# Optimization experiments

Measured on AMD Instinct MI355X. Metric: run time of the kernel, lower is better.

## Reference

```python
import jax, jax.numpy as jnp
import numpy as np


def setup_inputs() -> dict:
    key = jax.random.key(0)
    k1, k2, k3, k4, k5 = jax.random.split(key, 5)
    B, H, W, C = 4, 64, 64, 256
    d = C // 8
    return {
        "x": jax.random.normal(k1, (B, H, W, C), dtype=jnp.float32),
        "Wf": jax.random.normal(k2, (C, d), dtype=jnp.float32) * 0.05,
        "Wg": jax.random.normal(k3, (C, d), dtype=jnp.float32) * 0.05,
        "Wh": jax.random.normal(k4, (C, C), dtype=jnp.float32) * 0.05,
        "gamma": jax.random.normal(k5, (1,), dtype=jnp.float32),
    }


def reference(x, Wf, Wg, Wh, gamma):
    # x: [B,H,W,C]; 1x1 convs (no bias) == channel matmuls
    B, H, W, C = x.shape
    N = H * W
    f = jnp.einsum('bhwc,cd->bhwd', x, Wf).reshape(B, N, -1)  # keys  [B,N,d]
    g = jnp.einsum('bhwc,cd->bhwd', x, Wg).reshape(B, N, -1)  # query [B,N,d]
    h = jnp.einsum('bhwc,ce->bhwe', x, Wh).reshape(B, N, -1)  # value [B,N,C]
    s = jnp.einsum('bnd,bmd->bnm', g, f)       # [B,N,N], no 1/sqrt(d) scale (faithful)
    beta = jax.nn.softmax(s, axis=-1)
    o = jnp.einsum('bnm,bmc->bnc', beta, h).reshape(B, H, W, C)
    return gamma * o + x
```

## Files before the change

kernel.cpp:

```cpp
#include <hip/hip_runtime.h>
#include <math.h>

#define B_   4
#define N_   4096
#define C_   256
#define D_   32
#define QT   64
#define KTB  128
#define NT2  (N_/KTB)
#define L2E  1.4426950408889634f

typedef __attribute__((ext_vector_type(8)))  short  short8;
typedef __attribute__((ext_vector_type(4)))  float  f32x4;
typedef __attribute__((ext_vector_type(16))) float  f32x16;

__device__ __forceinline__ unsigned short f2bf(float f) {
    unsigned int u = __builtin_bit_cast(unsigned int, f);
    u += 0x7fffu + ((u >> 16) & 1u);
    return (unsigned short)(u >> 16);
}
__device__ __forceinline__ unsigned pack2(float lo, float hi) {
    return (unsigned)f2bf(lo) | ((unsigned)f2bf(hi) << 16);
}
__device__ __forceinline__ unsigned pack2rn(float lo, float hi) {
    unsigned ul = __builtin_bit_cast(unsigned, lo) + 0x8000u;
    unsigned uh = __builtin_bit_cast(unsigned, hi) + 0x8000u;
    return (ul >> 16) | (uh & 0xffff0000u);
}

__global__ __launch_bounds__(64) void wcast(const float* __restrict__ Wf,
        const float* __restrict__ Wg, const float* __restrict__ Wh,
        unsigned short* __restrict__ WT) {
    const int e = blockIdx.x;
    const int t = threadIdx.x;
    const float* src; int stride, col; float sc = 1.f;
    if (e < 256)      { src = Wh; stride = 256; col = e; }
    else if (e < 288) { src = Wf; stride = 32;  col = e - 256; }
    else              { src = Wg; stride = 32;  col = e - 288; sc = L2E; }
    const int c0 = t * 4;
    __align__(8) unsigned short tmp[4];
    #pragma unroll
    for (int i = 0; i < 4; ++i)
        tmp[i] = f2bf(src[(size_t)(c0 + i) * stride + col] * sc);
    *(uint2*)(WT + (size_t)e * 256 + c0) = *(const uint2*)tmp;
}

__global__ __launch_bounds__(256, 2) void proj(const float* __restrict__ x,
        const unsigned short* __restrict__ WT,
        unsigned short* __restrict__ f, unsigned short* __restrict__ g,
        unsigned short* __restrict__ hT) {
    __shared__ unsigned short xb[32 * 256];
    const int t = threadIdx.x;
    const int l = t & 63, w = t >> 6;
    const long n0 = (long)blockIdx.x * 32;
    const int b = (int)(n0 >> 12), nloc = (int)(n0 & 4095);

    {
        const int r = t >> 3, ch = (t & 7) * 32;
        const float* xp = x + (n0 + r) * C_ + ch;
        #pragma unroll
        for (int m4 = 0; m4 < 8; ++m4) {
            float4 v = *(const float4*)(xp + m4 * 4);
            unsigned u0 = pack2(v.x, v.y), u1 = pack2(v.z, v.w);
            const int byte = (r * 512 + (ch + m4 * 4) * 2) ^ ((r & 7) << 4);
            *(uint2*)((char*)xb + byte) = make_uint2(u0, u1);
        }
    }
    __syncthreads();

    const int l15 = l & 15, l31 = l & 31;
    const int l4 = (l >> 4) & 3, hi = (l >> 5) & 1;

    f32x16 acc0, acc1;
    #pragma unroll
    for (int i = 0; i < 16; ++i) { acc0[i] = 0.f; acc1[i] = 0.f; }
    const int e0 = w * 64 + l31;
    #pragma unroll
    for (int ks = 0; ks < 16; ++ks) {
        short8 A = *(const short8*)((const char*)xb +
                    ((l31 * 512 + ks * 32 + hi * 16) ^ ((l31 & 7) << 4)));
        short8 B0 = *(const short8*)(WT + (size_t)e0 * 256 + ks * 16 + hi * 8);
        short8 B1 = *(const short8*)(WT + (size_t)(e0 + 32) * 256 + ks * 16 + hi * 8);
        acc0 = __builtin_amdgcn_mfma_f32_32x32x16_bf16(A, B0, acc0, 0, 0, 0);
        acc1 = __builtin_amdgcn_mfma_f32_32x32x16_bf16(A, B1, acc1, 0, 0, 0);
    }
    f32x4 fgacc[2];
    #pragma unroll
    for (int rf = 0; rf < 2; ++rf)
        #pragma unroll
        for (int i = 0; i < 4; ++i) fgacc[rf][i] = 0.f;
    const int fcol = w * 16 + l15;
    #pragma unroll
    for (int ks2 = 0; ks2 < 8; ++ks2) {
        short8 Bf = *(const short8*)(WT + (size_t)(256 + fcol) * 256 + ks2 * 32 + l4 * 8);
        #pragma unroll
        for (int rf = 0; rf < 2; ++rf) {
            const int row = rf * 16 + l15;
            short8 A = *(const short8*)((const char*)xb +
                        ((row * 512 + ks2 * 64 + l4 * 16) ^ ((row & 7) << 4)));
            fgacc[rf] = __builtin_amdgcn_mfma_f32_16x16x32_bf16(A, Bf, fgacc[rf], 0, 0, 0);
        }
    }

    #pragma unroll
    for (int ef = 0; ef < 2; ++ef) {
        const f32x16& a = ef ? acc1 : acc0;
        const int e = e0 + ef * 32;
        unsigned short* dp = hT + ((size_t)b * C_ + e) * N_ + nloc + 4 * hi;
        #pragma unroll
        for (int qd = 0; qd < 4; ++qd) {
            unsigned u0 = pack2(a[4*qd+0], a[4*qd+1]);
            unsigned u1 = pack2(a[4*qd+2], a[4*qd+3]);
            *(uint2*)(dp + 8 * qd) = make_uint2(u0, u1);
        }
    }
    {
        unsigned short* outp = (fcol < 32) ? (f + fcol) : (g + fcol - 32);
        #pragma unroll
        for (int rf = 0; rf < 2; ++rf)
            #pragma unroll
            for (int r = 0; r < 4; ++r) {
                const int row = rf * 16 + l4 * 4 + r;
                outp[(size_t)(n0 + row) * D_] = f2bf(fgacc[rf][r]);
            }
    }
}

__global__ __launch_bounds__(512, 2) void attn(
        const unsigned short* __restrict__ g,
        const unsigned short* __restrict__ f,
        const unsigned short* __restrict__ hT,
        const float* __restrict__ x,
        const float* __restrict__ gammap,
        float* __restrict__ out) {

    __shared__ unsigned short P[2][QT * KTB];
    __shared__ float Lpart[8][4][16];
    __shared__ float linv[QT];

    const int bid = (int)blockIdx.x;
    const int s = (bid & 7) * 32 + (bid >> 3);
    const int q0 = (s & 63) * QT;
    const int b  = s >> 6;

    const int t = threadIdx.x, l = t & 63, w = t >> 6;
    const long nb = (long)b * N_;
    const unsigned short* hb = hT + (size_t)b * C_ * N_;

    {
        uint4* pz = (uint4*)&P[0][0];
        pz[t] = make_uint4(0,0,0,0);       pz[t+512]  = make_uint4(0,0,0,0);
        pz[t+1024] = make_uint4(0,0,0,0);  pz[t+1536] = make_uint4(0,0,0,0);
    }

    const int l15 = l & 15, l31 = l & 31;
    const int l4 = (l >> 4) & 3, hi = (l >> 5) & 1;

    short8 gB[4];
    #pragma unroll
    for (int qf = 0; qf < 4; ++qf)
        gB[qf] = *(const short8*)(g + (size_t)(nb + q0 + qf*16 + l15) * D_ + l4*8);

    const int ecol = w * 32 + l31;
    const unsigned short* hcol = hb + (size_t)ecol * N_ + hi * 8;
    const size_t fbase = (size_t)(nb + w*16 + l15) * D_ + l4*8;

    const int pwB = ((w*2 + (l4>>1))*64 + l15)*16 + (l4&1)*8;
    const int prB = hi*1024 + l31*16;

    float la[4] = {0.f, 0.f, 0.f, 0.f};
    f32x16 acc0, acc1;
    #pragma unroll
    for (int i = 0; i < 16; ++i) { acc0[i] = 0.f; acc1[i] = 0.f; }

    short8 fA[2], hB[2][8];
    fA[0] = *(const short8*)(f + fbase);
    fA[1] = *(const short8*)(f + fbase + (size_t)KTB * D_);
    #pragma unroll
    for (int kk = 0; kk < 8; ++kk) {
        hB[0][kk] = *(const short8*)(hcol + kk * 16);
        hB[1][kk] = *(const short8*)(hcol + (size_t)KTB + kk * 16);
    }

    f32x4 S[4];

#define QK(slot) { \
    f32x4 zz; zz[0]=0.f; zz[1]=0.f; zz[2]=0.f; zz[3]=0.f; \
    _Pragma("unroll") \
    for (int qf = 0; qf < 4; ++qf) \
        S[qf] = __builtin_amdgcn_mfma_f32_16x16x32_bf16(fA[slot], gB[qf], zz, 0,0,0); \
}

#define EXPAND(buf) { \
    _Pragma("unroll") \
    for (int qf = 0; qf < 4; ++qf) { \
        float p0 = exp2f(S[qf][0]); \
        float p1 = exp2f(S[qf][1]); \
        float p2 = exp2f(S[qf][2]); \
        float p3 = exp2f(S[qf][3]); \
        la[qf] += (p0+p1)+(p2+p3); \
        *(uint2*)((char*)&P[buf][0] + pwB + qf*256) = \
            make_uint2(pack2rn(p0,p1), pack2rn(p2,p3)); \
    } \
}

#define BODY(CUR, NXT, kvar, DO_N, DO_PF) { \
    __syncthreads(); \
    if (DO_N) QK(NXT); \
    _Pragma("unroll") \
    for (int kk = 0; kk < 8; ++kk) { \
        short8 a0 = *(const short8*)((const char*)&P[CUR][0] + kk*2048 + prB); \
        short8 a1 = *(const short8*)((const char*)&P[CUR][0] + kk*2048 + prB + 512); \
        acc0 = __builtin_amdgcn_mfma_f32_32x32x16_bf16(a0, hB[CUR][kk], acc0, 0,0,0); \
        acc1 = __builtin_amdgcn_mfma_f32_32x32x16_bf16(a1, hB[CUR][kk], acc1, 0,0,0); \
    } \
    if (DO_PF) { \
        const int ktp = ((kvar) + 2) & (NT2 - 1); \
        fA[CUR] = *(const short8*)(f + fbase + (size_t)ktp * KTB * D_); \
        _Pragma("unroll") \
        for (int kk = 0; kk < 8; ++kk) \
            hB[CUR][kk] = *(const short8*)(hcol + (size_t)ktp * KTB + kk * 16); \
    } \
    if (DO_N) EXPAND(NXT); \
}

    QK(0);
    __syncthreads();
    EXPAND(0);

    #pragma unroll 1
    for (int k = 0; k < NT2 - 2; k += 2) {
        BODY(0, 1, k,     true, true);
        BODY(1, 0, k + 1, true, true);
    }
    BODY(0, 1, NT2 - 2, true,  false);
    BODY(1, 0, NT2 - 1, false, false);
#undef BODY
#undef EXPAND
#undef QK

    #pragma unroll
    for (int qf = 0; qf < 4; ++qf) {
        la[qf] += __shfl_xor(la[qf], 16, 64);
        la[qf] += __shfl_xor(la[qf], 32, 64);
    }
    if (l < 16) {
        #pragma unroll
        for (int qf = 0; qf < 4; ++qf) Lpart[w][qf][l] = la[qf];
    }
    __syncthreads();
    if (t < QT) {
        const int qf = t >> 4, r = t & 15;
        float sm = 0.f;
        #pragma unroll
        for (int ww = 0; ww < 8; ++ww) sm += Lpart[ww][qf][r];
        linv[t] = 1.f / fmaxf(sm, 1e-30f);
    }
    __syncthreads();

    const float gamma = gammap[0];
    #pragma unroll
    for (int qh = 0; qh < 2; ++qh) {
        const f32x16& a = qh ? acc1 : acc0;
        #pragma unroll
        for (int reg = 0; reg < 16; ++reg) {
            const int row = qh*32 + (reg & 3) + 8*(reg >> 2) + 4*hi;
            const size_t o = (size_t)(nb + q0 + row) * C_ + ecol;
            out[o] = fmaf(gamma, a[reg] * linv[row], x[o]);
        }
    }
}

extern "C" void kernel_launch(void* const* d_in, const int* in_sizes, int n_in,
                              void* d_out, int out_size, void* d_ws, size_t ws_size,
                              hipStream_t stream) {
    const float* x     = (const float*)d_in[0];
    const float* Wf    = (const float*)d_in[1];
    const float* Wg    = (const float*)d_in[2];
    const float* Wh    = (const float*)d_in[3];
    const float* gamma = (const float*)d_in[4];
    float* out = (float*)d_out;

    unsigned short* WT  = (unsigned short*)d_ws;
    unsigned short* fb  = WT + 320 * 256;
    unsigned short* gb  = fb + (size_t)B_ * N_ * D_;
    unsigned short* hTb = gb + (size_t)B_ * N_ * D_;

    wcast<<<dim3(320), dim3(64), 0, stream>>>(Wf, Wg, Wh, WT);
    proj <<<dim3(B_ * N_ / 32), dim3(256), 0, stream>>>(x, WT, fb, gb, hTb);
    attn <<<dim3(256), dim3(512), 0, stream>>>(gb, fb, hTb, x, gamma, out);
}
```

Baseline: 95.37 us.

## Split attention work across 16 waves with single-buffered V prefetch

Doubles the attention block to 1024 threads so each wave handles half the query rows (2 q-fragments, one 32x32 accumulator) for its column slice. The V tile prefetch becomes single-buffered, issued one tile ahead, while keys stay two tiles ahead. The aim is to cut per-wave register pressure and raise wave-level parallelism for latency hiding. In exchange, each V column is loaded by two waves, and V-load latency is less hidden.

```diff
diff --git a/kernel.cpp b/kernel.cpp
--- a/kernel.cpp
+++ b/kernel.cpp
@@ -126,7 +126,7 @@
     }
 }
 
-__global__ __launch_bounds__(512, 2) void attn(
+__global__ __launch_bounds__(1024, 4) void attn(
         const unsigned short* __restrict__ g,
         const unsigned short* __restrict__ f,
         const unsigned short* __restrict__ hT,
@@ -135,7 +135,7 @@
         float* __restrict__ out) {
 
     __shared__ unsigned short P[2][QT * KTB];
-    __shared__ float Lpart[8][4][16];
+    __shared__ float Lpart[16][2][16];
     __shared__ float linv[QT];
 
     const int bid = (int)blockIdx.x;
@@ -149,125 +149,119 @@
 
     {
         uint4* pz = (uint4*)&P[0][0];
-        pz[t] = make_uint4(0,0,0,0);       pz[t+512]  = make_uint4(0,0,0,0);
-        pz[t+1024] = make_uint4(0,0,0,0);  pz[t+1536] = make_uint4(0,0,0,0);
+        pz[t] = make_uint4(0,0,0,0);
+        pz[t + 1024] = make_uint4(0,0,0,0);
     }
 
     const int l15 = l & 15, l31 = l & 31;
     const int l4 = (l >> 4) & 3, hi = (l >> 5) & 1;
-
-    short8 gB[4];
-    #pragma unroll
-    for (int qf = 0; qf < 4; ++qf)
-        gB[qf] = *(const short8*)(g + (size_t)(nb + q0 + qf*16 + l15) * D_ + l4*8);
-
-    const int ecol = w * 32 + l31;
+    const int kf = w & 7;
+    const int qp = (w >> 3) * 2;
+    const int qh = w >> 3;
+
+    short8 gB[2];
+    #pragma unroll
+    for (int j = 0; j < 2; ++j)
+        gB[j] = *(const short8*)(g + (size_t)(nb + q0 + (qp+j)*16 + l15) * D_ + l4*8);
+
+    const int ecol = (w & 7) * 32 + l31;
     const unsigned short* hcol = hb + (size_t)ecol * N_ + hi * 8;
-    const size_t fbase = (size_t)(nb + w*16 + l15) * D_ + l4*8;
-
-    const int pwB = ((w*2 + (l4>>1))*64 + l15)*16 + (l4&1)*8;
-    const int prB = hi*1024 + l31*16;
-
-    float la[4] = {0.f, 0.f, 0.f, 0.f};
-    f32x16 acc0, acc1;
-    #pragma unroll
-    for (int i = 0; i < 16; ++i) { acc0[i] = 0.f; acc1[i] = 0.f; }
-
-    short8 fA[2], hB[2][8];
-    fA[0] = *(const short8*)(f + fbase);
-    fA[1] = *(const short8*)(f + fbase + (size_t)KTB * D_);
-    #pragma unroll
-    for (int kk = 0; kk < 8; ++kk) {
-        hB[0][kk] = *(const short8*)(hcol + kk * 16);
-        hB[1][kk] = *(const short8*)(hcol + (size_t)KTB + kk * 16);
-    }
-
-    f32x4 S[4];
-
-#define QK(slot) { \
+    const size_t fbase = (size_t)(nb + kf*16 + l15) * D_ + l4*8;
+
+    const int pwB = ((kf*2 + (l4>>1))*64 + l15)*16 + (l4&1)*8 + qp*256;
+    const int prB = hi*1024 + qh*512 + l31*16;
+
+    float la0 = 0.f, la1 = 0.f;
+    f32x16 acc;
+    #pragma unroll
+    for (int i = 0; i < 16; ++i) acc[i] = 0.f;
+
+    short8 fA, hB[8];
+    fA = *(const short8*)(f + fbase);
+    #pragma unroll
+    for (int kk = 0; kk < 8; ++kk)
+        hB[kk] = *(const short8*)(hcol + kk * 16);
+
+    f32x4 S[2];
+
+#define QK() { \
     f32x4 zz; zz[0]=0.f; zz[1]=0.f; zz[2]=0.f; zz[3]=0.f; \
-    _Pragma("unroll") \
-    for (int qf = 0; qf < 4; ++qf) \
-        S[qf] = __builtin_amdgcn_mfma_f32_16x16x32_bf16(fA[slot], gB[qf], zz, 0,0,0); \
+    S[0] = __builtin_amdgcn_mfma_f32_16x16x32_bf16(fA, gB[0], zz, 0,0,0); \
+    S[1] = __builtin_amdgcn_mfma_f32_16x16x32_bf16(fA, gB[1], zz, 0,0,0); \
 }
 
 #define EXPAND(buf) { \
-    _Pragma("unroll") \
-    for (int qf = 0; qf < 4; ++qf) { \
-        float p0 = exp2f(S[qf][0]); \
-        float p1 = exp2f(S[qf][1]); \
-        float p2 = exp2f(S[qf][2]); \
-        float p3 = exp2f(S[qf][3]); \
-        la[qf] += (p0+p1)+(p2+p3); \
-        *(uint2*)((char*)&P[buf][0] + pwB + qf*256) = \
+    { \
+        float p0 = exp2f(S[0][0]), p1 = exp2f(S[0][1]); \
+        float p2 = exp2f(S[0][2]), p3 = exp2f(S[0][3]); \
+        la0 += (p0+p1)+(p2+p3); \
+        *(uint2*)((char*)&P[buf][0] + pwB) = \
+            make_uint2(pack2rn(p0,p1), pack2rn(p2,p3)); \
+    } \
+    { \
+        float p0 = exp2f(S[1][0]), p1 = exp2f(S[1][1]); \
+        float p2 = exp2f(S[1][2]), p3 = exp2f(S[1][3]); \
+        la1 += (p0+p1)+(p2+p3); \
+        *(uint2*)((char*)&P[buf][0] + pwB + 256) = \
             make_uint2(pack2rn(p0,p1), pack2rn(p2,p3)); \
     } \
 }
 
 #define BODY(CUR, NXT, kvar, DO_N, DO_PF) { \
     __syncthreads(); \
-    if (DO_N) QK(NXT); \
+    if (DO_N) QK(); \
     _Pragma("unroll") \
     for (int kk = 0; kk < 8; ++kk) { \
-        short8 a0 = *(const short8*)((const char*)&P[CUR][0] + kk*2048 + prB); \
-        short8 a1 = *(const short8*)((const char*)&P[CUR][0] + kk*2048 + prB + 512); \
-        acc0 = __builtin_amdgcn_mfma_f32_32x32x16_bf16(a0, hB[CUR][kk], acc0, 0,0,0); \
-        acc1 = __builtin_amdgcn_mfma_f32_32x32x16_bf16(a1, hB[CUR][kk], acc1, 0,0,0); \
+        short8 a = *(const short8*)((const char*)&P[CUR][0] + kk*2048 + prB); \
+        acc = __builtin_amdgcn_mfma_f32_32x32x16_bf16(a, hB[kk], acc, 0,0,0); \
     } \
     if (DO_PF) { \
-        const int ktp = ((kvar) + 2) & (NT2 - 1); \
-        fA[CUR] = *(const short8*)(f + fbase + (size_t)ktp * KTB * D_); \
+        const int kh = ((kvar) + 1) & (NT2 - 1); \
         _Pragma("unroll") \
         for (int kk = 0; kk < 8; ++kk) \
-            hB[CUR][kk] = *(const short8*)(hcol + (size_t)ktp * KTB + kk * 16); \
+            hB[kk] = *(const short8*)(hcol + (size_t)kh * KTB + kk * 16); \
+        const int kf2 = ((kvar) + 2) & (NT2 - 1); \
+        fA = *(const short8*)(f + fbase + (size_t)kf2 * KTB * D_); \
     } \
     if (DO_N) EXPAND(NXT); \
 }
 
-    QK(0);
+    QK();
+    fA = *(const short8*)(f + fbase + (size_t)KTB * D_);
     __syncthreads();
     EXPAND(0);
 
     #pragma unroll 1
     for (int k = 0; k < NT2 - 2; k += 2) {
         BODY(0, 1, k,     true, true);
-        BODY(1, 0, k + 1, true, true);
-    }
-    BODY(0, 1, NT2 - 2, true,  false);
+        BODY(1, 0, k + 1, true, (k + 1 < NT2 - 2));
+    }
+    BODY(0, 1, NT2 - 2, true,  true);
     BODY(1, 0, NT2 - 1, false, false);
 #undef BODY
 #undef EXPAND
 #undef QK
 
-    #pragma unroll
-    for (int qf = 0; qf < 4; ++qf) {
-        la[qf] += __shfl_xor(la[qf], 16, 64);
-        la[qf] += __shfl_xor(la[qf], 32, 64);
-    }
-    if (l < 16) {
-        #pragma unroll
-        for (int qf = 0; qf < 4; ++qf) Lpart[w][qf][l] = la[qf];
-    }
+    la0 += __shfl_xor(la0, 16, 64); la0 += __shfl_xor(la0, 32, 64);
+    la1 += __shfl_xor(la1, 16, 64); la1 += __shfl_xor(la1, 32, 64);
+    if (l < 16) { Lpart[w][0][l] = la0; Lpart[w][1][l] = la1; }
     __syncthreads();
     if (t < QT) {
         const int qf = t >> 4, r = t & 15;
+        const int p = qf >> 1, j = qf & 1;
         float sm = 0.f;
         #pragma unroll
-        for (int ww = 0; ww < 8; ++ww) sm += Lpart[ww][qf][r];
+        for (int i = 0; i < 8; ++i) sm += Lpart[p*8 + i][j][r];
         linv[t] = 1.f / fmaxf(sm, 1e-30f);
     }
     __syncthreads();
 
     const float gamma = gammap[0];
     #pragma unroll
-    for (int qh = 0; qh < 2; ++qh) {
-        const f32x16& a = qh ? acc1 : acc0;
-        #pragma unroll
-        for (int reg = 0; reg < 16; ++reg) {
-            const int row = qh*32 + (reg & 3) + 8*(reg >> 2) + 4*hi;
-            const size_t o = (size_t)(nb + q0 + row) * C_ + ecol;
-            out[o] = fmaf(gamma, a[reg] * linv[row], x[o]);
-        }
+    for (int reg = 0; reg < 16; ++reg) {
+        const int row = qh*32 + (reg & 3) + 8*(reg >> 2) + 4*hi;
+        const size_t o = (size_t)(nb + q0 + row) * C_ + ecol;
+        out[o] = fmaf(gamma, acc[reg] * linv[row], x[o]);
     }
 }
 
@@ -288,5 +282,5 @@
 
     wcast<<<dim3(320), dim3(64), 0, stream>>>(Wf, Wg, Wh, WT);
     proj <<<dim3(B_ * N_ / 32), dim3(256), 0, stream>>>(x, WT, fb, gb, hTb);
-    attn <<<dim3(256), dim3(512), 0, stream>>>(gb, fb, hTb, x, gamma, out);
-}
+    attn <<<dim3(256), dim3(1024), 0, stream>>>(gb, fb, hTb, x, gamma, out);
+}
```

Result: slower. 150.3 us (+57.6%).

## Specialize warps into QK/softmax producers and PV consumers

Applied to the files above, without the earlier changes.

Splits the 8 waves into 4 producer waves that compute QK scores, exponentiate and write P tiles to shared memory, and 4 consumer waves that run the P·V MFMAs over 64 output columns each. The intent is to overlap the exp/pack work with the PV matrix multiplies across waves instead of serialising them within each wave. Each consumer now holds four 32x32 accumulators and prefetches V in halves. This raises register pressure on consumers, leaves producer MFMA units idle, and risks load imbalance between the two roles.

```diff
diff --git a/kernel.cpp b/kernel.cpp
--- a/kernel.cpp
+++ b/kernel.cpp
@@ -135,7 +135,7 @@
         float* __restrict__ out) {
 
     __shared__ unsigned short P[2][QT * KTB];
-    __shared__ float Lpart[8][4][16];
+    __shared__ float Lpart[4][4][16];
     __shared__ float linv[QT];
 
     const int bid = (int)blockIdx.x;
@@ -155,118 +155,177 @@
 
     const int l15 = l & 15, l31 = l & 31;
     const int l4 = (l >> 4) & 3, hi = (l >> 5) & 1;
+    const bool isProd = (w < 4);
+    const int pw = w & 3;
+
+    float la[4] = {0.f, 0.f, 0.f, 0.f};
 
     short8 gB[4];
-    #pragma unroll
-    for (int qf = 0; qf < 4; ++qf)
-        gB[qf] = *(const short8*)(g + (size_t)(nb + q0 + qf*16 + l15) * D_ + l4*8);
-
-    const int ecol = w * 32 + l31;
-    const unsigned short* hcol = hb + (size_t)ecol * N_ + hi * 8;
-    const size_t fbase = (size_t)(nb + w*16 + l15) * D_ + l4*8;
-
-    const int pwB = ((w*2 + (l4>>1))*64 + l15)*16 + (l4&1)*8;
-    const int prB = hi*1024 + l31*16;
-
-    float la[4] = {0.f, 0.f, 0.f, 0.f};
-    f32x16 acc0, acc1;
-    #pragma unroll
-    for (int i = 0; i < 16; ++i) { acc0[i] = 0.f; acc1[i] = 0.f; }
-
-    short8 fA[2], hB[2][8];
-    fA[0] = *(const short8*)(f + fbase);
-    fA[1] = *(const short8*)(f + fbase + (size_t)KTB * D_);
-    #pragma unroll
-    for (int kk = 0; kk < 8; ++kk) {
-        hB[0][kk] = *(const short8*)(hcol + kk * 16);
-        hB[1][kk] = *(const short8*)(hcol + (size_t)KTB + kk * 16);
-    }
-
-    f32x4 S[4];
-
-#define QK(slot) { \
+    size_t fbase0 = 0, fbase1 = 0;
+    int pw0B = 0, pw1B = 0;
+    short8 fA_A[2], fA_B[2];
+    f32x4 S0[4], S1[4];
+
+    const unsigned short* hcol0 = nullptr;
+    const unsigned short* hcol1 = nullptr;
+    const int prB = hi * 1024 + l31 * 16;
+    short8 hB0[8], hB1[8];
+    f32x16 acc00, acc10, acc01, acc11;
+    #pragma unroll
+    for (int i = 0; i < 16; ++i) {
+        acc00[i] = 0.f; acc10[i] = 0.f; acc01[i] = 0.f; acc11[i] = 0.f;
+    }
+
+    if (isProd) {
+        #pragma unroll
+        for (int qf = 0; qf < 4; ++qf)
+            gB[qf] = *(const short8*)(g + (size_t)(nb + q0 + qf*16 + l15) * D_ + l4*8);
+        fbase0 = (size_t)(nb + (2*pw + 0)*16 + l15) * D_ + l4*8;
+        fbase1 = (size_t)(nb + (2*pw + 1)*16 + l15) * D_ + l4*8;
+        pw0B = (2*pw + 0)*2048 + (l4>>1)*1024 + l15*16 + (l4&1)*8;
+        pw1B = (2*pw + 1)*2048 + (l4>>1)*1024 + l15*16 + (l4&1)*8;
+    } else {
+        hcol0 = hb + (size_t)(pw*64 + l31) * N_ + hi * 8;
+        hcol1 = hcol0 + (size_t)32 * N_;
+    }
+
+#define PQK(FA) { \
     f32x4 zz; zz[0]=0.f; zz[1]=0.f; zz[2]=0.f; zz[3]=0.f; \
     _Pragma("unroll") \
-    for (int qf = 0; qf < 4; ++qf) \
-        S[qf] = __builtin_amdgcn_mfma_f32_16x16x32_bf16(fA[slot], gB[qf], zz, 0,0,0); \
-}
-
-#define EXPAND(buf) { \
-    _Pragma("unroll") \
     for (int qf = 0; qf < 4; ++qf) { \
-        float p0 = exp2f(S[qf][0]); \
-        float p1 = exp2f(S[qf][1]); \
-        float p2 = exp2f(S[qf][2]); \
-        float p3 = exp2f(S[qf][3]); \
+        S0[qf] = __builtin_amdgcn_mfma_f32_16x16x32_bf16(FA[0], gB[qf], zz, 0,0,0); \
+        S1[qf] = __builtin_amdgcn_mfma_f32_16x16x32_bf16(FA[1], gB[qf], zz, 0,0,0); \
+    } \
+}
+
+#define PEXP(buf) { \
+    _Pragma("unroll") \
+    for (int qf = 0; qf < 4; ++qf) { \
+        float p0 = exp2f(S0[qf][0]), p1 = exp2f(S0[qf][1]); \
+        float p2 = exp2f(S0[qf][2]), p3 = exp2f(S0[qf][3]); \
         la[qf] += (p0+p1)+(p2+p3); \
-        *(uint2*)((char*)&P[buf][0] + pwB + qf*256) = \
+        *(uint2*)((char*)&P[buf][0] + pw0B + qf*256) = \
             make_uint2(pack2rn(p0,p1), pack2rn(p2,p3)); \
     } \
-}
-
-#define BODY(CUR, NXT, kvar, DO_N, DO_PF) { \
-    __syncthreads(); \
-    if (DO_N) QK(NXT); \
-    _Pragma("unroll") \
-    for (int kk = 0; kk < 8; ++kk) { \
+    _Pragma("unroll") \
+    for (int qf = 0; qf < 4; ++qf) { \
+        float p0 = exp2f(S1[qf][0]), p1 = exp2f(S1[qf][1]); \
+        float p2 = exp2f(S1[qf][2]), p3 = exp2f(S1[qf][3]); \
+        la[qf] += (p0+p1)+(p2+p3); \
+        *(uint2*)((char*)&P[buf][0] + pw1B + qf*256) = \
+            make_uint2(pack2rn(p0,p1), pack2rn(p2,p3)); \
+    } \
+}
+
+#define CPV(CUR, ktn) { \
+    _Pragma("unroll") \
+    for (int kk = 0; kk < 4; ++kk) { \
         short8 a0 = *(const short8*)((const char*)&P[CUR][0] + kk*2048 + prB); \
         short8 a1 = *(const short8*)((const char*)&P[CUR][0] + kk*2048 + prB + 512); \
-        acc0 = __builtin_amdgcn_mfma_f32_32x32x16_bf16(a0, hB[CUR][kk], acc0, 0,0,0); \
-        acc1 = __builtin_amdgcn_mfma_f32_32x32x16_bf16(a1, hB[CUR][kk], acc1, 0,0,0); \
-    } \
-    if (DO_PF) { \
-        const int ktp = ((kvar) + 2) & (NT2 - 1); \
-        fA[CUR] = *(const short8*)(f + fbase + (size_t)ktp * KTB * D_); \
-        _Pragma("unroll") \
-        for (int kk = 0; kk < 8; ++kk) \
-            hB[CUR][kk] = *(const short8*)(hcol + (size_t)ktp * KTB + kk * 16); \
-    } \
-    if (DO_N) EXPAND(NXT); \
-}
-
-    QK(0);
+        acc00 = __builtin_amdgcn_mfma_f32_32x32x16_bf16(a0, hB0[kk], acc00, 0,0,0); \
+        acc10 = __builtin_amdgcn_mfma_f32_32x32x16_bf16(a1, hB0[kk], acc10, 0,0,0); \
+        acc01 = __builtin_amdgcn_mfma_f32_32x32x16_bf16(a0, hB1[kk], acc01, 0,0,0); \
+        acc11 = __builtin_amdgcn_mfma_f32_32x32x16_bf16(a1, hB1[kk], acc11, 0,0,0); \
+    } \
+    _Pragma("unroll") \
+    for (int kk = 0; kk < 4; ++kk) { \
+        hB0[kk] = *(const short8*)(hcol0 + (size_t)(ktn) * KTB + kk * 16); \
+        hB1[kk] = *(const short8*)(hcol1 + (size_t)(ktn) * KTB + kk * 16); \
+    } \
+    _Pragma("unroll") \
+    for (int kk = 4; kk < 8; ++kk) { \
+        short8 a0 = *(const short8*)((const char*)&P[CUR][0] + kk*2048 + prB); \
+        short8 a1 = *(const short8*)((const char*)&P[CUR][0] + kk*2048 + prB + 512); \
+        acc00 = __builtin_amdgcn_mfma_f32_32x32x16_bf16(a0, hB0[kk], acc00, 0,0,0); \
+        acc10 = __builtin_amdgcn_mfma_f32_32x32x16_bf16(a1, hB0[kk], acc10, 0,0,0); \
+        acc01 = __builtin_amdgcn_mfma_f32_32x32x16_bf16(a0, hB1[kk], acc01, 0,0,0); \
+        acc11 = __builtin_amdgcn_mfma_f32_32x32x16_bf16(a1, hB1[kk], acc11, 0,0,0); \
+    } \
+    _Pragma("unroll") \
+    for (int kk = 4; kk < 8; ++kk) { \
+        hB0[kk] = *(const short8*)(hcol0 + (size_t)(ktn) * KTB + kk * 16); \
+        hB1[kk] = *(const short8*)(hcol1 + (size_t)(ktn) * KTB + kk * 16); \
+    } \
+}
+
+#define BODY(CUR, NXT, kvar, FA, DO_N) { \
+    __syncthreads(); \
+    if (isProd) { \
+        if (DO_N) PQK(FA); \
+        { \
+            const int kt3 = ((kvar) + 3) & (NT2 - 1); \
+            FA[0] = *(const short8*)(f + fbase0 + (size_t)kt3 * KTB * D_); \
+            FA[1] = *(const short8*)(f + fbase1 + (size_t)kt3 * KTB * D_); \
+        } \
+        if (DO_N) PEXP(NXT); \
+    } else { \
+        const int ktn = ((kvar) + 1) & (NT2 - 1); \
+        CPV(CUR, ktn); \
+    } \
+}
+
     __syncthreads();
-    EXPAND(0);
+    if (isProd) {
+        short8 f0[2];
+        f0[0] = *(const short8*)(f + fbase0);
+        f0[1] = *(const short8*)(f + fbase1);
+        PQK(f0);
+        fA_A[0] = *(const short8*)(f + fbase0 + (size_t)1 * KTB * D_);
+        fA_A[1] = *(const short8*)(f + fbase1 + (size_t)1 * KTB * D_);
+        fA_B[0] = *(const short8*)(f + fbase0 + (size_t)2 * KTB * D_);
+        fA_B[1] = *(const short8*)(f + fbase1 + (size_t)2 * KTB * D_);
+        PEXP(0);
+    } else {
+        #pragma unroll
+        for (int kk = 0; kk < 8; ++kk) {
+            hB0[kk] = *(const short8*)(hcol0 + kk * 16);
+            hB1[kk] = *(const short8*)(hcol1 + kk * 16);
+        }
+    }
 
     #pragma unroll 1
     for (int k = 0; k < NT2 - 2; k += 2) {
-        BODY(0, 1, k,     true, true);
-        BODY(1, 0, k + 1, true, true);
-    }
-    BODY(0, 1, NT2 - 2, true,  false);
-    BODY(1, 0, NT2 - 1, false, false);
+        BODY(0, 1, k,     fA_A, true);
+        BODY(1, 0, k + 1, fA_B, true);
+    }
+    BODY(0, 1, NT2 - 2, fA_A, true);
+    BODY(1, 0, NT2 - 1, fA_B, false);
 #undef BODY
-#undef EXPAND
-#undef QK
+#undef CPV
+#undef PEXP
+#undef PQK
 
     #pragma unroll
     for (int qf = 0; qf < 4; ++qf) {
         la[qf] += __shfl_xor(la[qf], 16, 64);
         la[qf] += __shfl_xor(la[qf], 32, 64);
     }
-    if (l < 16) {
-        #pragma unroll
-        for (int qf = 0; qf < 4; ++qf) Lpart[w][qf][l] = la[qf];
+    if (isProd && l < 16) {
+        #pragma unroll
+        for (int qf = 0; qf < 4; ++qf) Lpart[pw][qf][l] = la[qf];
     }
     __syncthreads();
     if (t < QT) {
         const int qf = t >> 4, r = t & 15;
-        float sm = 0.f;
-        #pragma unroll
-        for (int ww = 0; ww < 8; ++ww) sm += Lpart[ww][qf][r];
+        const float sm = Lpart[0][qf][r] + Lpart[1][qf][r] +
+                         Lpart[2][qf][r] + Lpart[3][qf][r];
         linv[t] = 1.f / fmaxf(sm, 1e-30f);
     }
     __syncthreads();
 
-    const float gamma = gammap[0];
-    #pragma unroll
-    for (int qh = 0; qh < 2; ++qh) {
-        const f32x16& a = qh ? acc1 : acc0;
+    if (!isProd) {
+        const float gamma = gammap[0];
+        const int ec0 = pw * 64 + l31;
         #pragma unroll
         for (int reg = 0; reg < 16; ++reg) {
-            const int row = qh*32 + (reg & 3) + 8*(reg >> 2) + 4*hi;
-            const size_t o = (size_t)(nb + q0 + row) * C_ + ecol;
-            out[o] = fmaf(gamma, a[reg] * linv[row], x[o]);
+            const int r0 = (reg & 3) + 8 * (reg >> 2) + 4 * hi;
+            const int r1 = r0 + 32;
+            const size_t o00 = (size_t)(nb + q0 + r0) * C_ + ec0;
+            const size_t o10 = (size_t)(nb + q0 + r1) * C_ + ec0;
+            out[o00]      = fmaf(gamma, acc00[reg] * linv[r0], x[o00]);
+            out[o00 + 32] = fmaf(gamma, acc01[reg] * linv[r0], x[o00 + 32]);
+            out[o10]      = fmaf(gamma, acc10[reg] * linv[r1], x[o10]);
+            out[o10 + 32] = fmaf(gamma, acc11[reg] * linv[r1], x[o10 + 32]);
         }
     }
 }
```

New measurement: 105.8 us. +10.9%, slower.
